# Performance work log

Hardware: AMD Instinct MI355X
Metric: run time of the kernel (lower is better)

The kernel has to match this reference:

```python
import jax, jax.numpy as jnp
import numpy as np

D_MODEL = 1024
NHEAD = 16
HEAD_DIM = D_MODEL // NHEAD
DIM_FF = 4096
B, TC, TP = 4, 1024, 1024
EPS = 1e-5


def _layernorm(x, g, b):
    mu = jnp.mean(x, axis=-1, keepdims=True)
    var = jnp.mean(jnp.square(x - mu), axis=-1, keepdims=True)
    return (x - mu) * jax.lax.rsqrt(var + EPS) * g + b


def setup_inputs() -> dict:
    key = jax.random.key(0)
    ks = jax.random.split(key, 12)
    s = 0.02
    return {
        "x": jax.random.normal(ks[0], (B, TC, D_MODEL), jnp.float32),
        "Kp": jax.random.normal(ks[1], (B, NHEAD, TP, HEAD_DIM), jnp.float32),
        "Vp": jax.random.normal(ks[2], (B, NHEAD, TP, HEAD_DIM), jnp.float32),
        "pos_offset": TP,
        "wqkv": jax.random.normal(ks[3], (D_MODEL, 3 * D_MODEL), jnp.float32) * s,
        "bqkv": jnp.zeros((3 * D_MODEL,), jnp.float32),
        "wo": jax.random.normal(ks[4], (D_MODEL, D_MODEL), jnp.float32) * s,
        "bo": jnp.zeros((D_MODEL,), jnp.float32),
        "g1": jnp.ones((D_MODEL,), jnp.float32),
        "be1": jnp.zeros((D_MODEL,), jnp.float32),
        "g2": jnp.ones((D_MODEL,), jnp.float32),
        "be2": jnp.zeros((D_MODEL,), jnp.float32),
        "w1": jax.random.normal(ks[5], (D_MODEL, DIM_FF), jnp.float32) * s,
        "bf1": jnp.zeros((DIM_FF,), jnp.float32),
        "w2": jax.random.normal(ks[6], (DIM_FF, D_MODEL), jnp.float32) * s,
        "bf2": jnp.zeros((D_MODEL,), jnp.float32),
    }


def reference(x, Kp, Vp, pos_offset, wqkv, bqkv, wo, bo, g1, be1, g2, be2, w1, bf1, w2, bf2):
    Bsz, Tc, D = x.shape
    H, Dh = NHEAD, HEAD_DIM
    h = _layernorm(x, g1, be1)
    qkv = (h @ wqkv + bqkv).reshape(Bsz, Tc, 3, H, Dh).transpose(2, 0, 3, 1, 4)
    q, k_new, v_new = qkv[0], qkv[1], qkv[2]  # [B,H,Tc,Dh]
    K = jnp.concatenate([Kp, k_new], axis=2)  # [B,H,Tk,Dh]
    V = jnp.concatenate([Vp, v_new], axis=2)
    Tk = K.shape[2]
    scale = Dh ** -0.5
    # fused causal-masked attention; equivalent to the per-token loop:
    # query i attends keys j with j <= pos_offset + i
    scores = jnp.einsum("bhqd,bhkd->bhqk", q, K) * scale
    q_idx = jnp.arange(Tc)[:, None]
    k_idx = jnp.arange(Tk)[None, :]
    mask = k_idx <= (pos_offset + q_idx)  # [Tc,Tk]
    scores = jnp.where(mask, scores, jnp.finfo(scores.dtype).min)
    attn = jax.nn.softmax(scores, axis=-1)
    o = jnp.einsum("bhqk,bhkd->bhqd", attn, V)
    o = o.transpose(0, 2, 1, 3).reshape(Bsz, Tc, D)
    x = x + o @ wo + bo
    h2 = _layernorm(x, g2, be2)
    ff = jax.nn.gelu(h2 @ w1 + bf1, approximate=False) @ w2 + bf2
    x = x + ff
    return x, K, V
```

## Files before the change

### kernel.cpp

```cpp
#include <hip/hip_runtime.h>
#include <math.h>

#define DM   1024
#define NH   16
#define DH   64
#define DFF  4096
#define BSZ  4
#define TCC  1024
#define TPP  1024
#define TKK  2048
#define NTOK (BSZ*TCC)

typedef __attribute__((ext_vector_type(8))) short bf16x8;
typedef __attribute__((ext_vector_type(4))) float f32x4;

__device__ __forceinline__ unsigned short f2bf(float x) {
  union { float f; unsigned u; } v; v.f = x;
  unsigned r = v.u + 0x7fffu + ((v.u >> 16) & 1u);
  return (unsigned short)(r >> 16);
}
__device__ __forceinline__ unsigned pk2(float a, float b) {
  return (unsigned)f2bf(a) | ((unsigned)f2bf(b) << 16);
}

__device__ __forceinline__ void gload16(const void* g, void* l) {
  __builtin_amdgcn_global_load_lds(
      (const __attribute__((address_space(1))) void*)g,
      (__attribute__((address_space(3))) void*)l, 16, 0, 0);
}

__device__ __forceinline__ float wave_reduce_sum(float v) {
#pragma unroll
  for (int off = 32; off > 0; off >>= 1)
    v += __shfl_down(v, off, 64);
  return v;
}

__device__ __forceinline__ float gelu_f(float x) {
  float z = fabsf(x) * 0.70710678118654752440f;
  float t = 1.0f / (1.0f + 0.3275911f * z);
  float y = t * (0.254829592f +
            t * (-0.284496736f +
            t * (1.421413741f +
            t * (-1.453152027f +
            t * 1.061405429f))));
  float e = __expf(-z * z);
  float erfz = 1.0f - y * e;
  float s = (x >= 0.0f) ? erfz : -erfz;
  return 0.5f * x * (1.0f + s);
}

__global__ __launch_bounds__(256) void castT_kernel(
    const float* __restrict__ W, unsigned short* __restrict__ Wt, int K, int N) {
  __shared__ float tile[32][33];
  int nb = blockIdx.x << 5, kb = blockIdx.y << 5;
  int c = threadIdx.x & 31, r8 = threadIdx.x >> 5;
#pragma unroll
  for (int i = 0; i < 32; i += 8)
    tile[r8 + i][c] = W[(size_t)(kb + r8 + i) * N + nb + c];
  __syncthreads();
#pragma unroll
  for (int i = 0; i < 32; i += 8)
    Wt[(size_t)(nb + r8 + i) * K + kb + c] = f2bf(tile[c][r8 + i]);
}

__global__ __launch_bounds__(256) void castVt_kernel(
    const float* __restrict__ V, unsigned short* __restrict__ Vt) {
  __shared__ float tile[32][33];
  int z = blockIdx.z;
  const float* W = V + (size_t)z * TKK * DH;
  unsigned short* Wt = Vt + (size_t)z * DH * TKK;
  int nb = blockIdx.x << 5;
  int kb = blockIdx.y << 5;
  int c = threadIdx.x & 31, r8 = threadIdx.x >> 5;
#pragma unroll
  for (int i = 0; i < 32; i += 8)
    tile[r8 + i][c] = W[(size_t)(kb + r8 + i) * DH + nb + c];
  __syncthreads();
#pragma unroll
  for (int i = 0; i < 32; i += 8)
    Wt[(size_t)(nb + r8 + i) * TKK + kb + c] = f2bf(tile[c][r8 + i]);
}

__global__ __launch_bounds__(256) void copy_kv_kernel(
    const float4* __restrict__ Kp, const float4* __restrict__ Vp,
    float4* __restrict__ Kout, float4* __restrict__ Vout,
    unsigned short* __restrict__ Kbf) {
  int idx = blockIdx.x * 256 + threadIdx.x;
  int r = idx >> 4;
  int c = idx & 15;
  int dr = (r >> 10) * TKK + (r & 1023);
  float4 kv = Kp[idx];
  Kout[dr * 16 + c] = kv;
  Vout[dr * 16 + c] = Vp[idx];
  if (Kbf != nullptr) {
    uint2 pk;
    pk.x = pk2(kv.x, kv.y);
    pk.y = pk2(kv.z, kv.w);
    *(uint2*)(Kbf + (size_t)(dr * 16 + c) * 4) = pk;
  }
}

__global__ __launch_bounds__(256) void ln_kernel(
    const float* __restrict__ x, const float* __restrict__ g,
    const float* __restrict__ b, unsigned short* __restrict__ out) {
  __shared__ float red[8];
  int row = blockIdx.x;
  int tid = threadIdx.x;
  const float4* xr = (const float4*)(x + (size_t)row * DM);
  float4 xv = xr[tid];
  float s  = xv.x + xv.y + xv.z + xv.w;
  float ss = xv.x*xv.x + xv.y*xv.y + xv.z*xv.z + xv.w*xv.w;
  s  = wave_reduce_sum(s);
  ss = wave_reduce_sum(ss);
  int lane = tid & 63, wid = tid >> 6;
  if (lane == 0) { red[wid] = s; red[4 + wid] = ss; }
  __syncthreads();
  s  = red[0] + red[1] + red[2] + red[3];
  ss = red[4] + red[5] + red[6] + red[7];
  float mu  = s * (1.0f / DM);
  float var = ss * (1.0f / DM) - mu * mu;
  float rs  = rsqrtf(var + 1e-5f);
  float4 gv = ((const float4*)g)[tid];
  float4 bv = ((const float4*)b)[tid];
  ushort4 ov;
  ov.x = f2bf((xv.x - mu) * rs * gv.x + bv.x);
  ov.y = f2bf((xv.y - mu) * rs * gv.y + bv.y);
  ov.z = f2bf((xv.z - mu) * rs * gv.z + bv.z);
  ov.w = f2bf((xv.w - mu) * rs * gv.w + bv.w);
  *(ushort4*)&out[(size_t)row * DM + tid * 4] = ov;
}

template <int MODE>
__global__ __launch_bounds__(512) void mm8_kernel(
    const unsigned short* __restrict__ A, const unsigned short* __restrict__ Bt,
    const float* __restrict__ bias,
    float* __restrict__ outf, unsigned short* __restrict__ outb,
    float* __restrict__ Kc, float* __restrict__ Vc,
    unsigned short* __restrict__ Kbfp,
    int M, int N, int K) {
  __shared__ __align__(16) short lds[4][2][8192];
  int tid = threadIdx.x;
  int l = tid & 63, w = tid >> 6;
  int wr = w >> 2, wc = w & 3;
  int cidx = l & 15, rg = l >> 4;
  int m0 = blockIdx.y << 8, n0 = blockIdx.x << 8;

  int r0 = tid >> 2;
  int cb = (((tid & 3) ^ ((r0 >> 1) & 3)) << 4);
  const char* gA = (const char*)A + (size_t)(m0 + r0) * 2 * K + cb;
  const char* gB = (const char*)Bt + (size_t)(n0 + r0) * 2 * K + cb;
  size_t rskip = (size_t)128 * 2 * K;

  int xcs = ((rg ^ ((cidx >> 1) & 3)) << 4);
  int offA = (wr * 128 + cidx) * 64 + xcs;
  int offB = (wc * 64 + cidx) * 64 + xcs;

  f32x4 acc[8][4] = {};
  int NT = K >> 5;

  auto stage = [&](int t, int half) {
    char* la = (char*)&lds[t & 3][0][0] + tid * 16 + half * 8192;
    char* lb = (char*)&lds[t & 3][1][0] + tid * 16 + half * 8192;
    const char* sa = gA + t * 64 + (half ? rskip : 0);
    const char* sb = gB + t * 64 + (half ? rskip : 0);
    gload16(sa, la);
    gload16(sb, lb);
  };

  stage(0, 0); stage(0, 1);
  stage(1, 0); stage(1, 1);
  stage(2, 0); stage(2, 1);
  asm volatile("s_waitcnt vmcnt(8)" ::: "memory");
  __builtin_amdgcn_sched_barrier(0);
  __builtin_amdgcn_s_barrier();

  for (int t = 0; t < NT; ++t) {
    const char* pa = (const char*)&lds[t & 3][0][0];
    const char* pb = (const char*)&lds[t & 3][1][0];
    bf16x8 af[4], bg[4], a2[4];
#pragma unroll
    for (int i = 0; i < 4; ++i)
      af[i] = *(const bf16x8*)(pa + offA + i * 1024);
#pragma unroll
    for (int j = 0; j < 4; ++j)
      bg[j] = *(const bf16x8*)(pb + offB + j * 1024);
    if (t + 3 < NT) stage(t + 3, 0);
    __builtin_amdgcn_s_barrier();
    asm volatile("s_waitcnt lgkmcnt(0)" ::: "memory");
    __builtin_amdgcn_sched_barrier(0);
    __builtin_amdgcn_s_setprio(1);
#pragma unroll
    for (int i = 0; i < 4; ++i)
#pragma unroll
      for (int j = 0; j < 4; ++j)
        acc[i][j] = __builtin_amdgcn_mfma_f32_16x16x32_bf16(
            af[i], bg[j], acc[i][j], 0, 0, 0);
    __builtin_amdgcn_s_setprio(0);
    __builtin_amdgcn_s_barrier();
#pragma unroll
    for (int i = 0; i < 4; ++i)
      a2[i] = *(const bf16x8*)(pa + offA + (i + 4) * 1024);
    if (t + 3 < NT) stage(t + 3, 1);
    if (t + 3 < NT) {
      asm volatile("s_waitcnt vmcnt(8)" ::: "memory");
    } else if (t + 2 < NT) {
      asm volatile("s_waitcnt vmcnt(4)" ::: "memory");
    } else {
      asm volatile("s_waitcnt vmcnt(0)" ::: "memory");
    }
    __builtin_amdgcn_sched_barrier(0);
    __builtin_amdgcn_s_barrier();
    asm volatile("s_waitcnt lgkmcnt(0)" ::: "memory");
    __builtin_amdgcn_sched_barrier(0);
    __builtin_amdgcn_s_setprio(1);
#pragma unroll
    for (int i = 0; i < 4; ++i)
#pragma unroll
      for (int j = 0; j < 4; ++j)
        acc[i + 4][j] = __builtin_amdgcn_mfma_f32_16x16x32_bf16(
            a2[i], bg[j], acc[i + 4][j], 0, 0, 0);
    __builtin_amdgcn_s_setprio(0);
    __builtin_amdgcn_s_barrier();
  }

#pragma unroll
  for (int i = 0; i < 8; ++i) {
#pragma unroll
    for (int j = 0; j < 4; ++j) {
      int col = n0 + wc * 64 + j * 16 + cidx;
      float bb = bias[col];
#pragma unroll
      for (int r = 0; r < 4; ++r) {
        int row = m0 + wr * 128 + i * 16 + rg * 4 + r;
        float v = acc[i][j][r] + bb;
        if (MODE == 0) {
          int which = col >> 10, c = col & 1023;
          int hh = c >> 6, dd = c & 63;
          int b = row >> 10, tt = row & 1023;
          size_t base = (size_t)(b * NH + hh);
          if (which == 0)      outb[(base * TCC + tt) * DH + dd] = f2bf(v * 0.125f);
          else if (which == 1) {
            size_t off = (base * TKK + TPP + tt) * DH + dd;
            Kc[off] = v;
            if (Kbfp != nullptr) Kbfp[off] = f2bf(v);
          } else               Vc[(base * TKK + TPP + tt) * DH + dd] = v;
        } else {
          outb[(size_t)row * N + col] = f2bf(gelu_f(v));
        }
      }
    }
  }
}

template <int MODE, int DEPTH>
__global__ __launch_bounds__(256) void mm_kernel(
    const unsigned short* __restrict__ A, const unsigned short* __restrict__ Bt,
    const float* __restrict__ bias, const float* __restrict__ res,
    float* __restrict__ outf, unsigned short* __restrict__ outb,
    int M, int N, int K) {
  __shared__ __align__(16) short As[DEPTH * 128 * 32];
  __shared__ __align__(16) short Bs[DEPTH * 128 * 32];
  int tid = threadIdx.x;
  int w = tid >> 6, l = tid & 63;
  int m0 = blockIdx.y << 7, n0 = blockIdx.x << 7;
  int wm = (w >> 1) << 6, wn = (w & 1) << 6;
  int cidx = l & 15, rg = l >> 4;
  f32x4 acc[4][4] = {};

  int idx0 = w * 1024 + l * 16;
  int idx1 = idx0 + 4096;
  const char* gA0 = (const char*)A + (size_t)(m0 + (idx0 >> 6)) * 2 * K + (idx0 & 63);
  const char* gA1 = (const char*)A + (size_t)(m0 + (idx1 >> 6)) * 2 * K + (idx1 & 63);
  const char* gB0 = (const char*)Bt + (size_t)(n0 + (idx0 >> 6)) * 2 * K + (idx0 & 63);
  const char* gB1 = (const char*)Bt + (size_t)(n0 + (idx1 >> 6)) * 2 * K + (idx1 & 63);

  auto stage = [&](int bsel) {
    char* base_a = (char*)As + bsel * 8192;
    char* base_b = (char*)Bs + bsel * 8192;
    gload16(gA0, base_a + idx0); gload16(gA1, base_a + idx1);
    gload16(gB0, base_b + idx0); gload16(gB1, base_b + idx1);
    gA0 += 64; gA1 += 64; gB0 += 64; gB1 += 64;
  };
  auto compute = [&](int bsel) {
    const short* pa = As + bsel * 4096;
    const short* pb = Bs + bsel * 4096;
    bf16x8 af[4], bfr[4];
#pragma unroll
    for (int i = 0; i < 4; ++i) {
      af[i]  = *(const bf16x8*)&pa[(wm + i * 16 + cidx) * 32 + rg * 8];
      bfr[i] = *(const bf16x8*)&pb[(wn + i * 16 + cidx) * 32 + rg * 8];
    }
#pragma unroll
    for (int i = 0; i < 4; ++i)
#pragma unroll
      for (int j = 0; j < 4; ++j)
        acc[i][j] = __builtin_amdgcn_mfma_f32_16x16x32_bf16(
            af[i], bfr[j], acc[i][j], 0, 0, 0);
  };

  int nt = K >> 5;
  if (DEPTH == 2) {
    stage(0);
    for (int t = 0; t < nt - 1; ++t) {
      __syncthreads();
      stage((t + 1) & 1);
      compute(t & 1);
    }
    __syncthreads();
    compute((nt - 1) & 1);
  } else {
    stage(0); stage(1); stage(2);
    for (int t = 0; t < nt - 3; ++t) {
      asm volatile("s_waitcnt vmcnt(8)" ::: "memory");
      __builtin_amdgcn_sched_barrier(0);
      __builtin_amdgcn_s_barrier();
      __builtin_amdgcn_sched_barrier(0);
      stage((t + 3) & 3);
      compute(t & 3);
    }
    asm volatile("s_waitcnt vmcnt(8)" ::: "memory");
    __builtin_amdgcn_sched_barrier(0);
    __builtin_amdgcn_s_barrier();
    __builtin_amdgcn_sched_barrier(0);
    compute((nt - 3) & 3);
    asm volatile("s_waitcnt vmcnt(4)" ::: "memory");
    __builtin_amdgcn_sched_barrier(0);
    __builtin_amdgcn_s_barrier();
    __builtin_amdgcn_sched_barrier(0);
    compute((nt - 2) & 3);
    asm volatile("s_waitcnt vmcnt(0)" ::: "memory");
    __builtin_amdgcn_sched_barrier(0);
    __builtin_amdgcn_s_barrier();
    __builtin_amdgcn_sched_barrier(0);
    compute((nt - 1) & 3);
  }

#pragma unroll
  for (int i = 0; i < 4; ++i) {
#pragma unroll
    for (int j = 0; j < 4; ++j) {
      int col = n0 + wn + j * 16 + cidx;
      float bb = bias[col];
#pragma unroll
      for (int r = 0; r < 4; ++r) {
        int row = m0 + wm + i * 16 + rg * 4 + r;
        float v = acc[i][j][r] + bb;
        if (MODE == 1) {
          size_t off = (size_t)row * N + col;
          outf[off] = res[off] + v;
        } else {
          outb[(size_t)row * N + col] = f2bf(gelu_f(v));
        }
      }
    }
  }
}

template <int KBF>
__global__ __launch_bounds__(256) void attn_kernel(
    const unsigned short* __restrict__ Qb, const float* __restrict__ K,
    const unsigned short* __restrict__ Kb16,
    const unsigned short* __restrict__ Vtb, const int* __restrict__ posp,
    unsigned short* __restrict__ o) {
  __shared__ __align__(16) unsigned short Qs[64][72];
  __shared__ __align__(16) unsigned short Ks[64][72];
  __shared__ __align__(16) unsigned short Vts[64][72];
  __shared__ __align__(16) unsigned short Pw[4][16][72];
  int tid = threadIdx.x;
  int w = tid >> 6, lane = tid & 63;
  int l15 = lane & 15, quad = lane >> 4;
  int blk = blockIdx.x;
  int bh = blk >> 4;
  int qbase = (blk & 15) << 6;
  int b = bh >> 4, h = bh & 15;
  int pos = *posp;

  {
    int r = tid >> 2, cg = (tid & 3) << 4;
    const unsigned short* src = Qb + ((size_t)bh * TCC + qbase + r) * DH + cg;
    *(uint4*)&Qs[r][cg]     = *(const uint4*)src;
    *(uint4*)&Qs[r][cg + 8] = *(const uint4*)(src + 8);
  }
  __syncthreads();
  bf16x8 aq0 = *(const bf16x8*)&Qs[16 * w + l15][quad * 8];
  bf16x8 aq1 = *(const bf16x8*)&Qs[16 * w + l15][32 + quad * 8];

  f32x4 accO[4] = {};
  f32x4 accL = {};
  bf16x8 ones;
#pragma unroll
  for (int i = 0; i < 8; ++i) ones[i] = (short)0x3F80;

  int nk = pos + qbase + 64; if (nk > TKK) nk = TKK;
  int ntiles = nk >> 6;
  const float* Kbh = K + (size_t)bh * TKK * DH;
  const unsigned short* Kbh16 = Kb16 + (size_t)bh * TKK * DH;
  const unsigned short* Vbh = Vtb + (size_t)bh * DH * TKK;

  for (int t = 0; t < ntiles; ++t) {
    int kt = t << 6;
    {
      int r = tid >> 2, cg = (tid & 3) << 4;
      if (KBF) {
        const unsigned short* ks = Kbh16 + (size_t)(kt + r) * DH + cg;
        *(uint4*)&Ks[r][cg]     = *(const uint4*)ks;
        *(uint4*)&Ks[r][cg + 8] = *(const uint4*)(ks + 8);
      } else {
        const float* ks = Kbh + (size_t)(kt + r) * DH + cg;
        float4 k0 = *(const float4*)ks,       k1 = *(const float4*)(ks + 4);
        float4 k2 = *(const float4*)(ks + 8), k3 = *(const float4*)(ks + 12);
        uint4 p0, p1;
        p0.x = pk2(k0.x, k0.y); p0.y = pk2(k0.z, k0.w);
        p0.z = pk2(k1.x, k1.y); p0.w = pk2(k1.z, k1.w);
        p1.x = pk2(k2.x, k2.y); p1.y = pk2(k2.z, k2.w);
        p1.z = pk2(k3.x, k3.y); p1.w = pk2(k3.z, k3.w);
        *(uint4*)&Ks[r][cg]     = p0;
        *(uint4*)&Ks[r][cg + 8] = p1;
      }
      const unsigned short* vs = Vbh + (size_t)r * TKK + kt + cg;
      *(uint4*)&Vts[r][cg]     = *(const uint4*)vs;
      *(uint4*)&Vts[r][cg + 8] = *(const uint4*)(vs + 8);
    }
    __syncthreads();
    f32x4 accS[4] = {};
    __builtin_amdgcn_s_setprio(1);
#pragma unroll
    for (int j = 0; j < 4; ++j) {
      bf16x8 bk0 = *(const bf16x8*)&Ks[16 * j + l15][quad * 8];
      bf16x8 bk1 = *(const bf16x8*)&Ks[16 * j + l15][32 + quad * 8];
      accS[j] = __builtin_amdgcn_mfma_f32_16x16x32_bf16(aq0, bk0, accS[j], 0, 0, 0);
      accS[j] = __builtin_amdgcn_mfma_f32_16x16x32_bf16(aq1, bk1, accS[j], 0, 0, 0);
    }
    __builtin_amdgcn_s_setprio(0);
    bool edge = (kt + 63 > pos + qbase);
#pragma unroll
    for (int j = 0; j < 4; ++j) {
      int key = kt + 16 * j + l15;
#pragma unroll
      for (int r = 0; r < 4; ++r) {
        float p = __expf(accS[j][r]);
        if (edge && key > pos + qbase + 16 * w + quad * 4 + r) p = 0.f;
        Pw[w][quad * 4 + r][16 * j + l15] = f2bf(p);
      }
    }
    bf16x8 ap0 = *(const bf16x8*)&Pw[w][l15][quad * 8];
    bf16x8 ap1 = *(const bf16x8*)&Pw[w][l15][32 + quad * 8];
    __builtin_amdgcn_s_setprio(1);
    accL = __builtin_amdgcn_mfma_f32_16x16x32_bf16(ap0, ones, accL, 0, 0, 0);
    accL = __builtin_amdgcn_mfma_f32_16x16x32_bf16(ap1, ones, accL, 0, 0, 0);
#pragma unroll
    for (int j2 = 0; j2 < 4; ++j2) {
      bf16x8 bv0 = *(const bf16x8*)&Vts[16 * j2 + l15][quad * 8];
      bf16x8 bv1 = *(const bf16x8*)&Vts[16 * j2 + l15][32 + quad * 8];
      accO[j2] = __builtin_amdgcn_mfma_f32_16x16x32_bf16(ap0, bv0, accO[j2], 0, 0, 0);
      accO[j2] = __builtin_amdgcn_mfma_f32_16x16x32_bf16(ap1, bv1, accO[j2], 0, 0, 0);
    }
    __builtin_amdgcn_s_setprio(0);
    __syncthreads();
  }
#pragma unroll
  for (int r = 0; r < 4; ++r) {
    float inv = 1.0f / accL[r];
    int qg = qbase + 16 * w + quad * 4 + r;
    size_t base = (((size_t)(b * TCC + qg)) * NH + h) * DH;
#pragma unroll
    for (int j2 = 0; j2 < 4; ++j2)
      o[base + 16 * j2 + l15] = f2bf(accO[j2][r] * inv);
  }
}

extern "C" void kernel_launch(void* const* d_in, const int* in_sizes, int n_in,
                              void* d_out, int out_size, void* d_ws, size_t ws_size,
                              hipStream_t stream) {
  (void)in_sizes; (void)n_in; (void)out_size;
  const float* x    = (const float*)d_in[0];
  const float* Kp   = (const float*)d_in[1];
  const float* Vp   = (const float*)d_in[2];
  const int*   posp = (const int*)d_in[3];
  const float* wqkv = (const float*)d_in[4];
  const float* bqkv = (const float*)d_in[5];
  const float* wo   = (const float*)d_in[6];
  const float* bo   = (const float*)d_in[7];
  const float* g1   = (const float*)d_in[8];
  const float* be1  = (const float*)d_in[9];
  const float* g2   = (const float*)d_in[10];
  const float* be2  = (const float*)d_in[11];
  const float* w1   = (const float*)d_in[12];
  const float* bf1  = (const float*)d_in[13];
  const float* w2   = (const float*)d_in[14];
  const float* bf2  = (const float*)d_in[15];

  float* xout = (float*)d_out;
  float* Kout = xout + (size_t)BSZ * TCC * DM;
  float* Vout = Kout + (size_t)BSZ * NH * TKK * DH;

  const size_t MB = 1024 * 1024;
  char* ws = (char*)d_ws;
  unsigned short* wqkvT = (unsigned short*)(ws);
  unsigned short* woT   = (unsigned short*)(ws + 6 * MB);
  unsigned short* w1T   = (unsigned short*)(ws + 8 * MB);
  unsigned short* w2T   = (unsigned short*)(ws + 16 * MB);
  unsigned short* hbf   = (unsigned short*)(ws + 24 * MB);
  unsigned short* ffbf  = (unsigned short*)(ws + 32 * MB);
  unsigned short* Qbuf  = (unsigned short*)(ws + 32 * MB);
  unsigned short* obf   = (unsigned short*)(ws + 40 * MB);
  unsigned short* Vtb   = (unsigned short*)(ws + 48 * MB);
  float*          x2    = xout;
  unsigned short* Kbf   = (ws_size >= 80 * MB)
                            ? (unsigned short*)(ws + 64 * MB) : nullptr;

  castT_kernel<<<dim3(96, 32),  dim3(256), 0, stream>>>(wqkv, wqkvT, DM, 3 * DM);
  castT_kernel<<<dim3(32, 32),  dim3(256), 0, stream>>>(wo,   woT,   DM, DM);
  castT_kernel<<<dim3(128, 32), dim3(256), 0, stream>>>(w1,   w1T,   DM, DFF);
  castT_kernel<<<dim3(32, 128), dim3(256), 0, stream>>>(w2,   w2T,   DFF, DM);

  copy_kv_kernel<<<dim3(4096), dim3(256), 0, stream>>>(
      (const float4*)Kp, (const float4*)Vp, (float4*)Kout, (float4*)Vout, Kbf);
  ln_kernel<<<dim3(NTOK), dim3(256), 0, stream>>>(x, g1, be1, hbf);
  mm8_kernel<0><<<dim3(12, 16), dim3(512), 0, stream>>>(
      hbf, wqkvT, bqkv, nullptr, Qbuf, Kout, Vout, Kbf, NTOK, 3 * DM, DM);
  castVt_kernel<<<dim3(2, 64, 64), dim3(256), 0, stream>>>(Vout, Vtb);
  if (Kbf != nullptr)
    attn_kernel<1><<<dim3(1024), dim3(256), 0, stream>>>(Qbuf, Kout, Kbf, Vtb, posp, obf);
  else
    attn_kernel<0><<<dim3(1024), dim3(256), 0, stream>>>(Qbuf, Kout, Kbf, Vtb, posp, obf);
  mm_kernel<1, 4><<<dim3(8, 32), dim3(256), 0, stream>>>(
      obf, woT, bo, x, x2, nullptr, NTOK, DM, DM);
  ln_kernel<<<dim3(NTOK), dim3(256), 0, stream>>>(x2, g2, be2, hbf);
  mm8_kernel<2><<<dim3(16, 16), dim3(512), 0, stream>>>(
      hbf, w1T, bf1, nullptr, ffbf, nullptr, nullptr, nullptr, NTOK, DFF, DM);
  mm_kernel<1, 4><<<dim3(8, 32), dim3(256), 0, stream>>>(
      ffbf, w2T, bf2, x2, xout, nullptr, NTOK, DM, DFF);
}
```

Baseline: 483.5 us.

## Use split-K 256x256 MFMA GEMM with atomic accumulation for N=1024 projections

Adds a split-K mode to the 256x256 tile bf16 MFMA GEMM. Each z-slice handles a quarter of K and atomically adds its partial sums into fp32 outputs zeroed by memset, with bias and residual added only by slice 0. It is used for the output projection and the FFN down-projection when the workspace is large enough, giving 256 blocks of larger tiles instead of 128x128 tiles. This trades two memsets and atomic read-modify-write traffic, plus non-deterministic summation order, for better tile reuse and more parallelism over K. x2 moves into workspace so the second split-K GEMM can accumulate into a zeroed xout.

Measured after the change: 584.1 us. +20.8%, slower.

```diff
diff --git a/kernel.cpp b/kernel.cpp
--- a/kernel.cpp
+++ b/kernel.cpp
@@ -131,10 +131,10 @@
   *(ushort4*)&out[(size_t)row * DM + tid * 4] = ov;
 }
 
-template <int MODE>
+template <int MODE, int NSPLIT>
 __global__ __launch_bounds__(512) void mm8_kernel(
     const unsigned short* __restrict__ A, const unsigned short* __restrict__ Bt,
-    const float* __restrict__ bias,
+    const float* __restrict__ bias, const float* __restrict__ res,
     float* __restrict__ outf, unsigned short* __restrict__ outb,
     float* __restrict__ Kc, float* __restrict__ Vc,
     unsigned short* __restrict__ Kbfp,
@@ -145,11 +145,13 @@
   int wr = w >> 2, wc = w & 3;
   int cidx = l & 15, rg = l >> 4;
   int m0 = blockIdx.y << 8, n0 = blockIdx.x << 8;
+  int z = (NSPLIT > 1) ? blockIdx.z : 0;
+  int KS = K / NSPLIT;
 
   int r0 = tid >> 2;
   int cb = (((tid & 3) ^ ((r0 >> 1) & 3)) << 4);
-  const char* gA = (const char*)A + (size_t)(m0 + r0) * 2 * K + cb;
-  const char* gB = (const char*)Bt + (size_t)(n0 + r0) * 2 * K + cb;
+  const char* gA = (const char*)A + (size_t)(m0 + r0) * 2 * K + cb + (size_t)2 * z * KS;
+  const char* gB = (const char*)Bt + (size_t)(n0 + r0) * 2 * K + cb + (size_t)2 * z * KS;
   size_t rskip = (size_t)128 * 2 * K;
 
   int xcs = ((rg ^ ((cidx >> 1) & 3)) << 4);
@@ -157,7 +159,7 @@
   int offB = (wc * 64 + cidx) * 64 + xcs;
 
   f32x4 acc[8][4] = {};
-  int NT = K >> 5;
+  int NT = KS >> 5;
 
   auto stage = [&](int t, int half) {
     char* la = (char*)&lds[t & 3][0][0] + tid * 16 + half * 8192;
@@ -245,8 +247,13 @@
             Kc[off] = v;
             if (Kbfp != nullptr) Kbfp[off] = f2bf(v);
           } else               Vc[(base * TKK + TPP + tt) * DH + dd] = v;
+        } else if (MODE == 2) {
+          outb[(size_t)row * N + col] = f2bf(gelu_f(v));
         } else {
-          outb[(size_t)row * N + col] = f2bf(gelu_f(v));
+          size_t off = (size_t)row * N + col;
+          float add = acc[i][j][r];
+          if (z == 0) add += bb + res[off];
+          unsafeAtomicAdd(&outf[off], add);
         }
       }
     }
@@ -300,41 +307,30 @@
   };
 
   int nt = K >> 5;
-  if (DEPTH == 2) {
-    stage(0);
-    for (int t = 0; t < nt - 1; ++t) {
-      __syncthreads();
-      stage((t + 1) & 1);
-      compute(t & 1);
-    }
-    __syncthreads();
-    compute((nt - 1) & 1);
-  } else {
-    stage(0); stage(1); stage(2);
-    for (int t = 0; t < nt - 3; ++t) {
-      asm volatile("s_waitcnt vmcnt(8)" ::: "memory");
-      __builtin_amdgcn_sched_barrier(0);
-      __builtin_amdgcn_s_barrier();
-      __builtin_amdgcn_sched_barrier(0);
-      stage((t + 3) & 3);
-      compute(t & 3);
-    }
+  stage(0); stage(1); stage(2);
+  for (int t = 0; t < nt - 3; ++t) {
     asm volatile("s_waitcnt vmcnt(8)" ::: "memory");
     __builtin_amdgcn_sched_barrier(0);
     __builtin_amdgcn_s_barrier();
     __builtin_amdgcn_sched_barrier(0);
-    compute((nt - 3) & 3);
-    asm volatile("s_waitcnt vmcnt(4)" ::: "memory");
-    __builtin_amdgcn_sched_barrier(0);
-    __builtin_amdgcn_s_barrier();
-    __builtin_amdgcn_sched_barrier(0);
-    compute((nt - 2) & 3);
-    asm volatile("s_waitcnt vmcnt(0)" ::: "memory");
-    __builtin_amdgcn_sched_barrier(0);
-    __builtin_amdgcn_s_barrier();
-    __builtin_amdgcn_sched_barrier(0);
-    compute((nt - 1) & 3);
-  }
+    stage((t + 3) & 3);
+    compute(t & 3);
+  }
+  asm volatile("s_waitcnt vmcnt(8)" ::: "memory");
+  __builtin_amdgcn_sched_barrier(0);
+  __builtin_amdgcn_s_barrier();
+  __builtin_amdgcn_sched_barrier(0);
+  compute((nt - 3) & 3);
+  asm volatile("s_waitcnt vmcnt(4)" ::: "memory");
+  __builtin_amdgcn_sched_barrier(0);
+  __builtin_amdgcn_s_barrier();
+  __builtin_amdgcn_sched_barrier(0);
+  compute((nt - 2) & 3);
+  asm volatile("s_waitcnt vmcnt(0)" ::: "memory");
+  __builtin_amdgcn_sched_barrier(0);
+  __builtin_amdgcn_s_barrier();
+  __builtin_amdgcn_sched_barrier(0);
+  compute((nt - 1) & 3);
 
 #pragma unroll
   for (int i = 0; i < 4; ++i) {
@@ -346,12 +342,8 @@
       for (int r = 0; r < 4; ++r) {
         int row = m0 + wm + i * 16 + rg * 4 + r;
         float v = acc[i][j][r] + bb;
-        if (MODE == 1) {
-          size_t off = (size_t)row * N + col;
-          outf[off] = res[off] + v;
-        } else {
-          outb[(size_t)row * N + col] = f2bf(gelu_f(v));
-        }
+        size_t off = (size_t)row * N + col;
+        outf[off] = res[off] + v;
       }
     }
   }
@@ -506,9 +498,15 @@
   unsigned short* Qbuf  = (unsigned short*)(ws + 32 * MB);
   unsigned short* obf   = (unsigned short*)(ws + 40 * MB);
   unsigned short* Vtb   = (unsigned short*)(ws + 48 * MB);
-  float*          x2    = xout;
   unsigned short* Kbf   = (ws_size >= 80 * MB)
                             ? (unsigned short*)(ws + 64 * MB) : nullptr;
+  bool big = (ws_size >= 96 * MB);
+  float* x2 = big ? (float*)(ws + 80 * MB) : xout;
+
+  if (big) {
+    hipMemsetAsync(x2,   0, (size_t)NTOK * DM * sizeof(float), stream);
+    hipMemsetAsync(xout, 0, (size_t)NTOK * DM * sizeof(float), stream);
+  }
 
   castT_kernel<<<dim3(96, 32),  dim3(256), 0, stream>>>(wqkv, wqkvT, DM, 3 * DM);
   castT_kernel<<<dim3(32, 32),  dim3(256), 0, stream>>>(wo,   woT,   DM, DM);
@@ -518,18 +516,29 @@
   copy_kv_kernel<<<dim3(4096), dim3(256), 0, stream>>>(
       (const float4*)Kp, (const float4*)Vp, (float4*)Kout, (float4*)Vout, Kbf);
   ln_kernel<<<dim3(NTOK), dim3(256), 0, stream>>>(x, g1, be1, hbf);
-  mm8_kernel<0><<<dim3(12, 16), dim3(512), 0, stream>>>(
-      hbf, wqkvT, bqkv, nullptr, Qbuf, Kout, Vout, Kbf, NTOK, 3 * DM, DM);
+  mm8_kernel<0, 1><<<dim3(12, 16), dim3(512), 0, stream>>>(
+      hbf, wqkvT, bqkv, nullptr, nullptr, Qbuf, Kout, Vout, Kbf, NTOK, 3 * DM, DM);
   castVt_kernel<<<dim3(2, 64, 64), dim3(256), 0, stream>>>(Vout, Vtb);
   if (Kbf != nullptr)
     attn_kernel<1><<<dim3(1024), dim3(256), 0, stream>>>(Qbuf, Kout, Kbf, Vtb, posp, obf);
   else
     attn_kernel<0><<<dim3(1024), dim3(256), 0, stream>>>(Qbuf, Kout, Kbf, Vtb, posp, obf);
-  mm_kernel<1, 4><<<dim3(8, 32), dim3(256), 0, stream>>>(
-      obf, woT, bo, x, x2, nullptr, NTOK, DM, DM);
-  ln_kernel<<<dim3(NTOK), dim3(256), 0, stream>>>(x2, g2, be2, hbf);
-  mm8_kernel<2><<<dim3(16, 16), dim3(512), 0, stream>>>(
-      hbf, w1T, bf1, nullptr, ffbf, nullptr, nullptr, nullptr, NTOK, DFF, DM);
-  mm_kernel<1, 4><<<dim3(8, 32), dim3(256), 0, stream>>>(
-      ffbf, w2T, bf2, x2, xout, nullptr, NTOK, DM, DFF);
-}
+
+  if (big) {
+    mm8_kernel<3, 4><<<dim3(4, 16, 4), dim3(512), 0, stream>>>(
+        obf, woT, bo, x, x2, nullptr, nullptr, nullptr, nullptr, NTOK, DM, DM);
+    ln_kernel<<<dim3(NTOK), dim3(256), 0, stream>>>(x2, g2, be2, hbf);
+    mm8_kernel<2, 1><<<dim3(16, 16), dim3(512), 0, stream>>>(
+        hbf, w1T, bf1, nullptr, nullptr, ffbf, nullptr, nullptr, nullptr, NTOK, DFF, DM);
+    mm8_kernel<3, 4><<<dim3(4, 16, 4), dim3(512), 0, stream>>>(
+        ffbf, w2T, bf2, x2, xout, nullptr, nullptr, nullptr, nullptr, NTOK, DM, DFF);
+  } else {
+    mm_kernel<1, 4><<<dim3(8, 32), dim3(256), 0, stream>>>(
+        obf, woT, bo, x, x2, nullptr, NTOK, DM, DM);
+    ln_kernel<<<dim3(NTOK), dim3(256), 0, stream>>>(x2, g2, be2, hbf);
+    mm8_kernel<2, 1><<<dim3(16, 16), dim3(512), 0, stream>>>(
+        hbf, w1T, bf1, nullptr, nullptr, ffbf, nullptr, nullptr, nullptr, NTOK, DFF, DM);
+    mm_kernel<1, 4><<<dim3(8, 32), dim3(256), 0, stream>>>(
+        ffbf, w2T, bf2, x2, xout, nullptr, NTOK, DM, DFF);
+  }
+}
```
